# Optimization experiments

Hardware: AMD Instinct MI355X
Metric: run time of the kernel (lower is better)

## Reference

```python
import jax, jax.numpy as jnp
import numpy as np

EMBED = 1024
HEADS = 16
HEAD_DIM = EMBED // HEADS
EPS = 1e-5  # torch LayerNorm default


def setup_inputs() -> dict:
    key = jax.random.key(0)
    ks = jax.random.split(key, 11)
    s = 1.0 / np.sqrt(EMBED)
    def lin(kw, kb):
        W = jax.random.uniform(kw, (EMBED, EMBED), jnp.float32, -s, s)
        b = jax.random.uniform(kb, (EMBED,), jnp.float32, -s, s)
        return W, b
    Wq, bq = lin(ks[0], ks[1])
    Wk, bk = lin(ks[2], ks[3])
    Wv, bv = lin(ks[4], ks[5])
    Wo, bo = lin(ks[6], ks[7])
    x = jax.random.normal(ks[8], (2, 2048, EMBED), jnp.float32)
    gamma = jnp.ones((EMBED,), jnp.float32)
    beta = jnp.zeros((EMBED,), jnp.float32)
    return {"x": x, "Wq": Wq, "bq": bq, "Wk": Wk, "bk": bk,
            "Wv": Wv, "bv": bv, "Wo": Wo, "bo": bo,
            "gamma": gamma, "beta": beta}


def _attn(x, Wq, bq, Wk, bk, Wv, bv, Wo, bo, gamma, beta):
    N, S, _ = x.shape
    # torch Linear: y = x @ W.T + b
    q = (x @ Wq.T + bq).reshape(N, S, HEADS, HEAD_DIM).transpose(0, 2, 1, 3)
    k = (x @ Wk.T + bk).reshape(N, S, HEADS, HEAD_DIM).transpose(0, 2, 1, 3)
    v = (x @ Wv.T + bv).reshape(N, S, HEADS, HEAD_DIM).transpose(0, 2, 1, 3)
    energy = jnp.einsum("bhqd,bhkd->bhqk", q, k) / np.sqrt(HEAD_DIM)
    causal = jnp.tril(jnp.ones((S, S), bool))  # [S,S]
    energy = jnp.where(causal[None, None], energy, -jnp.inf)
    attn = jax.nn.softmax(energy, axis=-1)
    out = jnp.einsum("bhqk,bhkd->bhqd", attn, v)
    out = out.transpose(0, 2, 1, 3).reshape(N, S, EMBED)
    out = out @ Wo.T + bo
    # residual + LayerNorm
    h = out + x
    mu = jnp.mean(h, axis=-1, keepdims=True)
    var = jnp.var(h, axis=-1, keepdims=True)
    return (h - mu) * jax.lax.rsqrt(var + EPS) * gamma + beta


def reference(x, Wq, bq, Wk, bk, Wv, bv, Wo, bo, gamma, beta):
    return _attn(x, Wq, bq, Wk, bk, Wv, bv, Wo, bo, gamma, beta)
```

## Files before the change

### kernel.cpp

```cpp
#include <hip/hip_runtime.h>

typedef __attribute__((ext_vector_type(8))) short short8;
typedef __attribute__((ext_vector_type(4))) float f32x4;
typedef __attribute__((ext_vector_type(4))) short short4v;

template<bool B> struct BoolC { static constexpr bool value = B; };

__device__ __forceinline__ short f2bs(float f) {
    union { float f; unsigned u; } c; c.f = f;
    unsigned r = 0x7FFFu + ((c.u >> 16) & 1u);
    return (short)((c.u + r) >> 16);
}

__device__ __forceinline__ unsigned fbits(float f) {
    union { float f; unsigned u; } c; c.f = f; return c.u;
}

__device__ __forceinline__ float fast_exp2(float x) {
    float r;
    asm("v_exp_f32 %0, %1" : "=v"(r) : "v"(x));
    return r;
}

__device__ __forceinline__ void gld_lds16(const void* g, void* l) {
    __builtin_amdgcn_global_load_lds(
        (const __attribute__((address_space(1))) unsigned int*)g,
        (__attribute__((address_space(3))) unsigned int*)l, 16, 0, 0);
}

__device__ __forceinline__ f32x4 mfma16(short8 a, short8 b, f32x4 c) {
    return __builtin_amdgcn_mfma_f32_16x16x32_bf16(a, b, c, 0, 0, 0);
}

template<int N> __device__ __forceinline__ void vmwait() {
    if constexpr (N == 0)      asm volatile("s_waitcnt vmcnt(0)" ::: "memory");
    else if constexpr (N == 3) asm volatile("s_waitcnt vmcnt(3)" ::: "memory");
    else if constexpr (N == 4) asm volatile("s_waitcnt vmcnt(4)" ::: "memory");
}

__global__ __launch_bounds__(256) void cvtall_kernel(
    const float* __restrict__ x,
    const float* __restrict__ Wq, const float* __restrict__ Wk,
    const float* __restrict__ Wv, const float* __restrict__ Wo,
    short* __restrict__ xb, short* __restrict__ wqkv, short* __restrict__ wob)
{
    int i = blockIdx.x * 256 + threadIdx.x;
    const float* src; short* dst; int off;
    if (i < 1048576) { src = x; dst = xb; off = i; }
    else {
        int j = i - 1048576, which = j >> 18;
        off = j & 262143;
        src = which == 0 ? Wq : (which == 1 ? Wk : (which == 2 ? Wv : Wo));
        dst = which == 3 ? wob : (wqkv + (size_t)which * 1048576);
    }
    float4 v = ((const float4*)src)[off];
    short4v o;
    o.x = f2bs(v.x); o.y = f2bs(v.y); o.z = f2bs(v.z); o.w = f2bs(v.w);
    ((short4v*)dst)[off] = o;
}

#define BN 128
#define BK 32

template<int MODE, int BMt>
__global__ __launch_bounds__(256) void gemm_bt(
    const short* __restrict__ A, const short* __restrict__ B,
    int M, int N, int K,
    const float* __restrict__ b0, const float* __restrict__ b1, const float* __restrict__ b2,
    short* __restrict__ oq, short* __restrict__ ok_, short* __restrict__ ov,
    const float* __restrict__ bo, const float* __restrict__ xres,
    float* __restrict__ outf)
{
    constexpr int IM = BMt / 32;
    constexpr int BUFSZ = (BMt + BN) * BK;
    constexpr int LPS = (BMt == 128) ? 4 : 3;
    __shared__ __align__(16) short SM[3 * BUFSZ];
    const int tid = threadIdx.x;
    const int wave = tid >> 6, lane = tid & 63;
    const int lhi = lane >> 4, llo = lane & 15;
    const int row0 = blockIdx.x * BMt, col0 = blockIdx.y * BN;
    const int wr = (wave >> 1) * (BMt / 2), wc = (wave & 1) * 64;

    f32x4 acc[IM][4] = {};

    const short* gA0 = A + (size_t)(row0 + (tid >> 2)) * K + (tid & 3) * 8;
    const short* gA1 = A + (size_t)(row0 + 64 + (tid >> 2)) * K + (tid & 3) * 8;
    const short* gB0 = B + (size_t)(col0 + (tid >> 2)) * K + (tid & 3) * 8;
    const short* gB1 = B + (size_t)(col0 + 64 + (tid >> 2)) * K + (tid & 3) * 8;

    auto stage = [&](int kk, int bf) {
        short* As = SM + bf * BUFSZ;
        short* Bs = As + BMt * BK;
        gld_lds16(gA0 + kk, &As[wave * 512]);
        if constexpr (BMt == 128) gld_lds16(gA1 + kk, &As[2048 + wave * 512]);
        gld_lds16(gB0 + kk, &Bs[wave * 512]);
        gld_lds16(gB1 + kk, &Bs[2048 + wave * 512]);
    };

    const int NT = K / BK;
    stage(0, 0);
    stage(BK, 1);

    for (int kt = 0; kt < NT; ++kt) {
        if (kt < NT - 1) vmwait<LPS>(); else vmwait<0>();
        __builtin_amdgcn_s_barrier();
        __builtin_amdgcn_sched_barrier(0);
        if (kt + 2 < NT) stage((kt + 2) * BK, (kt + 2) % 3);
        const short* As = SM + (kt % 3) * BUFSZ;
        const short* Bs = As + BMt * BK;
        short8 af[IM], bfr[4];
        #pragma unroll
        for (int i = 0; i < IM; ++i)
            af[i] = *(const short8*)&As[(wr + i * 16 + llo) * BK + lhi * 8];
        #pragma unroll
        for (int j = 0; j < 4; ++j)
            bfr[j] = *(const short8*)&Bs[(wc + j * 16 + llo) * BK + lhi * 8];
        #pragma unroll
        for (int i = 0; i < IM; ++i)
            #pragma unroll
            for (int j = 0; j < 4; ++j)
                acc[i][j] = mfma16(af[i], bfr[j], acc[i][j]);
    }

    if constexpr (MODE == 0) {
        const int which = (int)blockIdx.y >> 3;
        if (which < 2) {
            const float* bia = which == 0 ? b0 : b1;
            short* dst = which == 0 ? oq : ok_;
            #pragma unroll
            for (int i = 0; i < IM; ++i)
                #pragma unroll
                for (int j = 0; j < 4; ++j)
                    #pragma unroll
                    for (int r = 0; r < 4; ++r) {
                        int m = row0 + wr + i * 16 + lhi * 4 + r;
                        int nn = (col0 & 1023) + wc + j * 16 + llo;
                        float v = acc[i][j][r] + bia[nn];
                        int h = nn >> 6, d = nn & 63;
                        int bb = m >> 11, s = m & 2047;
                        dst[((size_t)((bb * 16 + h) * 2048 + s)) * 64 + d] = f2bs(v);
                    }
        } else {
            __syncthreads();
            short* T = SM + wave * (64 * 26);
            const int nn0 = (col0 - 2048) + wc;
            const int h = nn0 >> 6;
            const int bb = row0 >> 11;
            const int s0 = (row0 & 2047) + wr;
            short* vdst = ov + ((size_t)(bb * 16 + h) * 64) * 2048;
            #pragma unroll
            for (int i = 0; i < IM; ++i) {
                #pragma unroll
                for (int j = 0; j < 4; ++j) {
                    const float bias = b2[nn0 + j * 16 + llo];
                    unsigned u01 = __builtin_amdgcn_perm(fbits(acc[i][j][1] + bias),
                                                         fbits(acc[i][j][0] + bias), 0x07060302u);
                    unsigned u23 = __builtin_amdgcn_perm(fbits(acc[i][j][3] + bias),
                                                         fbits(acc[i][j][2] + bias), 0x07060302u);
                    unsigned* Tw = (unsigned*)&T[(j * 16 + llo) * 26];
                    Tw[lhi * 2]     = u01;
                    Tw[lhi * 2 + 1] = u23;
                }
                short8 a0 = *(const short8*)&T[lane * 26];
                short8 a1 = *(const short8*)&T[lane * 26 + 8];
                *(short8*)&vdst[(size_t)lane * 2048 + s0 + i * 16]     = a0;
                *(short8*)&vdst[(size_t)lane * 2048 + s0 + i * 16 + 8] = a1;
            }
        }
    } else {
        #pragma unroll
        for (int i = 0; i < IM; ++i)
            #pragma unroll
            for (int j = 0; j < 4; ++j)
                #pragma unroll
                for (int r = 0; r < 4; ++r) {
                    int m = row0 + wr + i * 16 + lhi * 4 + r;
                    int n = col0 + wc + j * 16 + llo;
                    size_t idx = (size_t)m * N + n;
                    outf[idx] = acc[i][j][r] + bo[n] + xres[idx];
                }
    }
}

#define SCL 0.18033688011f

__global__ __launch_bounds__(256) void attn_kernel(
    const short* __restrict__ Q, const short* __restrict__ K,
    const short* __restrict__ Vt, short* __restrict__ O)
{
    const int id = blockIdx.x;
    const int u = id >> 3;
    const int bh = (id & 7) * 4 + (u & 3);
    const int s4 = u >> 2;
    const int p = (s4 < 8) ? (2 * s4) : (31 - 2 * s4);
    const int q0L = p * 64, q0H = (31 - p) * 64;
    const int ntH = 32 - p;

    const short* Qb = Q  + (size_t)bh * 2048 * 64;
    const short* Kb = K  + (size_t)bh * 2048 * 64;
    const short* Vb = Vt + (size_t)bh * 64 * 2048;

    __shared__ __align__(16) short Ks[2][64 * 64];
    __shared__ __align__(16) short Vs[2][64 * 64];
    __shared__ __align__(16) short Ps[4][2][16 * 68];

    const int tid = threadIdx.x, wave = tid >> 6, lane = tid & 63;
    const int lhi = lane >> 4, llo = lane & 15;
    const int qwL = q0L + wave * 16, qwH = q0H + wave * 16;
    const int qgL = qwL + llo, qgH = qwH + llo;

    auto scale8 = [](short8 a) {
        short8 r;
        #pragma unroll
        for (int i = 0; i < 8; ++i) {
            union { unsigned u; float f; } c; c.u = ((unsigned)(unsigned short)a[i]) << 16;
            r[i] = f2bs(c.f * SCL);
        }
        return r;
    };
    const short8 qfL0 = scale8(*(const short8*)&Qb[(size_t)(qwL + llo) * 64 + lhi * 8]);
    const short8 qfL1 = scale8(*(const short8*)&Qb[(size_t)(qwL + llo) * 64 + 32 + lhi * 8]);
    const short8 qfH0 = scale8(*(const short8*)&Qb[(size_t)(qwH + llo) * 64 + lhi * 8]);
    const short8 qfH1 = scale8(*(const short8*)&Qb[(size_t)(qwH + llo) * 64 + 32 + lhi * 8]);

    const int tr = tid >> 3, tc = tid & 7, sc = tc ^ (tr & 7);
    const short* kS0 = Kb + (size_t)tr * 64 + sc * 8;
    const short* kS1 = Kb + (size_t)(32 + tr) * 64 + sc * 8;
    const short* vS0 = Vb + (size_t)tr * 2048 + sc * 8;
    const short* vS1 = Vb + (size_t)(32 + tr) * 2048 + sc * 8;
    const int dOff = wave * 512;

    f32x4 oL[4] = {}, oH[4] = {};
    float lL = 0.f, lH = 0.f;

    unsigned* PwH = (unsigned*)Ps[wave][0] + llo * 34;
    unsigned* PwL = (unsigned*)Ps[wave][1] + llo * 34;

    gld_lds16(kS0, Ks[0] + dOff);
    gld_lds16(kS1, Ks[0] + 2048 + dOff);
    gld_lds16(vS0, Vs[0] + dOff);
    gld_lds16(vS1, Vs[0] + 2048 + dOff);
    __syncthreads();

    const int swq = (llo & 7) << 3;

    auto smx = [&](f32x4 (&st)[4], float& lrow, unsigned* Pw, int qg, int kk0, bool diag) {
        if (diag) {
            #pragma unroll
            for (int t = 0; t < 4; ++t)
                #pragma unroll
                for (int j = 0; j < 4; ++j)
                    if (kk0 + t * 16 + lhi * 4 + j > qg) st[t][j] = -1e30f;
        }
        float rs0 = 0.f, rs1 = 0.f;
        #pragma unroll
        for (int t = 0; t < 4; ++t) {
            st[t][0] = fast_exp2(st[t][0]);
            st[t][1] = fast_exp2(st[t][1]);
            st[t][2] = fast_exp2(st[t][2]);
            st[t][3] = fast_exp2(st[t][3]);
            rs0 += st[t][0] + st[t][2];
            rs1 += st[t][1] + st[t][3];
        }
        lrow += rs0 + rs1;
        #pragma unroll
        for (int t = 0; t < 4; ++t) {
            Pw[t * 8 + lhi * 2]     = __builtin_amdgcn_perm(fbits(st[t][1]), fbits(st[t][0]), 0x07060302u);
            Pw[t * 8 + lhi * 2 + 1] = __builtin_amdgcn_perm(fbits(st[t][3]), fbits(st[t][2]), 0x07060302u);
        }
    };

    int cur = 0;
    auto tile = [&](int kt, auto dualc) {
        constexpr bool DUAL = decltype(dualc)::value;
        const int kk0 = kt * 64;
        if (kt + 1 < ntH) {
            const int nk = kk0 + 64;
            gld_lds16(kS0 + (size_t)nk * 64, Ks[cur ^ 1] + dOff);
            gld_lds16(kS1 + (size_t)nk * 64, Ks[cur ^ 1] + 2048 + dOff);
            gld_lds16(vS0 + nk, Vs[cur ^ 1] + dOff);
            gld_lds16(vS1 + nk, Vs[cur ^ 1] + 2048 + dOff);
        }

        f32x4 stH[4], stL[4];
        __builtin_amdgcn_s_setprio(1);
        #pragma unroll
        for (int t = 0; t < 4; ++t) {
            const int row = t * 16 + llo;
            short8 kf0 = *(const short8*)&Ks[cur][row * 64 + ((lhi * 8) ^ swq)];
            short8 kf1 = *(const short8*)&Ks[cur][row * 64 + ((lhi * 8 + 32) ^ swq)];
            f32x4 a = {};
            a = mfma16(kf0, qfH0, a);
            stH[t] = mfma16(kf1, qfH1, a);
            if (DUAL) {
                f32x4 b = {};
                b = mfma16(kf0, qfL0, b);
                stL[t] = mfma16(kf1, qfL1, b);
            }
        }
        __builtin_amdgcn_s_setprio(0);

        smx(stH, lH, PwH, qgH, kk0, kt == ntH - 1);
        if (DUAL) smx(stL, lL, PwL, qgL, kk0, kt == p);

        const short8 pH0 = *(const short8*)&Ps[wave][0][llo * 68 + lhi * 8];
        const short8 pH1 = *(const short8*)&Ps[wave][0][llo * 68 + 32 + lhi * 8];
        short8 pL0, pL1;
        if (DUAL) {
            pL0 = *(const short8*)&Ps[wave][1][llo * 68 + lhi * 8];
            pL1 = *(const short8*)&Ps[wave][1][llo * 68 + 32 + lhi * 8];
        }
        __builtin_amdgcn_s_setprio(1);
        #pragma unroll
        for (int dt = 0; dt < 4; ++dt) {
            const int row = dt * 16 + llo;
            short8 vf0 = *(const short8*)&Vs[cur][row * 64 + ((lhi * 8) ^ swq)];
            short8 vf1 = *(const short8*)&Vs[cur][row * 64 + ((lhi * 8 + 32) ^ swq)];
            oH[dt] = mfma16(pH0, vf0, oH[dt]);
            oH[dt] = mfma16(pH1, vf1, oH[dt]);
            if (DUAL) {
                oL[dt] = mfma16(pL0, vf0, oL[dt]);
                oL[dt] = mfma16(pL1, vf1, oL[dt]);
            }
        }
        __builtin_amdgcn_s_setprio(0);

        if (kt + 1 < ntH) __syncthreads();
        cur ^= 1;
    };

    for (int kt = 0; kt <= p; ++kt)      tile(kt, BoolC<true>{});
    for (int kt = p + 1; kt < ntH; ++kt) tile(kt, BoolC<false>{});

    lH += __shfl_xor(lH, 16); lH += __shfl_xor(lH, 32);
    lL += __shfl_xor(lL, 16); lL += __shfl_xor(lL, 32);
    const int b = bh >> 4, h = bh & 15;
    const float invH = 1.f / lH, invL = 1.f / lL;
    #pragma unroll
    for (int j = 0; j < 4; ++j) {
        const float ivH = __shfl(invH, lhi * 4 + j);
        const float ivL = __shfl(invL, lhi * 4 + j);
        const size_t rowH = (size_t)(b * 2048 + qwH + lhi * 4 + j);
        const size_t rowL = (size_t)(b * 2048 + qwL + lhi * 4 + j);
        #pragma unroll
        for (int dt = 0; dt < 4; ++dt) {
            int d = dt * 16 + llo;
            O[rowH * 1024 + h * 64 + d] = f2bs(oH[dt][j] * ivH);
            O[rowL * 1024 + h * 64 + d] = f2bs(oL[dt][j] * ivL);
        }
    }
}

__global__ __launch_bounds__(256) void ln_kernel(float* __restrict__ out,
        const float* __restrict__ gamma, const float* __restrict__ beta)
{
    const int row = blockIdx.x;
    float* p = out + (size_t)row * 1024;
    const int tid = threadIdx.x;
    float4 v = ((const float4*)p)[tid];
    float s = v.x + v.y + v.z + v.w;
    float ss = v.x * v.x + v.y * v.y + v.z * v.z + v.w * v.w;
    #pragma unroll
    for (int d = 1; d < 64; d <<= 1) {
        s  += __shfl_xor(s, d);
        ss += __shfl_xor(ss, d);
    }
    __shared__ float red[8];
    const int wave = tid >> 6, lane = tid & 63;
    if (lane == 0) { red[wave] = s; red[4 + wave] = ss; }
    __syncthreads();
    s  = red[0] + red[1] + red[2] + red[3];
    ss = red[4] + red[5] + red[6] + red[7];
    const float mu = s * (1.0f / 1024.0f);
    const float var = ss * (1.0f / 1024.0f) - mu * mu;
    const float rstd = rsqrtf(var + 1e-5f);
    float4 g = ((const float4*)gamma)[tid];
    float4 b = ((const float4*)beta)[tid];
    v.x = (v.x - mu) * rstd * g.x + b.x;
    v.y = (v.y - mu) * rstd * g.y + b.y;
    v.z = (v.z - mu) * rstd * g.z + b.z;
    v.w = (v.w - mu) * rstd * g.w + b.w;
    ((float4*)p)[tid] = v;
}

extern "C" void kernel_launch(void* const* d_in, const int* in_sizes, int n_in,
                              void* d_out, int out_size, void* d_ws, size_t ws_size,
                              hipStream_t stream)
{
    const float* x  = (const float*)d_in[0];
    const float* Wq = (const float*)d_in[1];
    const float* bq = (const float*)d_in[2];
    const float* Wk = (const float*)d_in[3];
    const float* bk = (const float*)d_in[4];
    const float* Wv = (const float*)d_in[5];
    const float* bv = (const float*)d_in[6];
    const float* Wo = (const float*)d_in[7];
    const float* bo = (const float*)d_in[8];
    const float* gamma = (const float*)d_in[9];
    const float* beta  = (const float*)d_in[10];
    float* out = (float*)d_out;

    char* ws = (char*)d_ws;
    short* xb   = (short*)(ws);
    short* wqkv = (short*)(ws + (8ull  << 20));
    short* wob  = (short*)(ws + (14ull << 20));
    short* qb   = (short*)(ws + (16ull << 20));
    short* kb   = (short*)(ws + (24ull << 20));
    short* vtb  = (short*)(ws + (32ull << 20));
    short* ab   = xb;

    cvtall_kernel<<<8192, 256, 0, stream>>>(x, Wq, Wk, Wv, Wo, xb, wqkv, wob);

    gemm_bt<0, 128><<<dim3(32, 24), 256, 0, stream>>>(xb, wqkv, 4096, 3072, 1024,
        bq, bk, bv, qb, kb, vtb, nullptr, nullptr, nullptr);

    attn_kernel<<<512, 256, 0, stream>>>(qb, kb, vtb, ab);

    gemm_bt<1, 64><<<dim3(64, 8), 256, 0, stream>>>(ab, wob, 4096, 1024, 1024,
        nullptr, nullptr, nullptr, nullptr, nullptr, nullptr, bo, x, out);

    ln_kernel<<<4096, 256, 0, stream>>>(out, gamma, beta);
}
```

Baseline: 111.2 us.

## Restructure attention to one query tile per block with split-K wave partitioning

Replaces the paired low/high query-tile scheduling (512 blocks) with one 64-row query tile per block (1024 blocks, heaviest tiles first). Within a block, waves split the work 2x2 across key halves and query halves, keep P in registers instead of staging through LDS, and combine the partial outputs and row sums through shared memory at the end. The intent is more parallelism and no per-tile LDS round-trip for P. In exchange it adds a cross-wave reduction and more blocks with uneven work.

```diff
diff --git a/kernel.cpp b/kernel.cpp
--- a/kernel.cpp
+++ b/kernel.cpp
@@ -3,8 +3,6 @@
 typedef __attribute__((ext_vector_type(8))) short short8;
 typedef __attribute__((ext_vector_type(4))) float f32x4;
 typedef __attribute__((ext_vector_type(4))) short short4v;
-
-template<bool B> struct BoolC { static constexpr bool value = B; };
 
 __device__ __forceinline__ short f2bs(float f) {
     union { float f; unsigned u; } c; c.f = f;
@@ -189,25 +187,23 @@
     const short* __restrict__ Vt, short* __restrict__ O)
 {
     const int id = blockIdx.x;
-    const int u = id >> 3;
-    const int bh = (id & 7) * 4 + (u & 3);
-    const int s4 = u >> 2;
-    const int p = (s4 < 8) ? (2 * s4) : (31 - 2 * s4);
-    const int q0L = p * 64, q0H = (31 - p) * 64;
-    const int ntH = 32 - p;
+    const int bh = (id & 7) * 4 + (id >> 8);
+    const int qt = 31 - ((id >> 3) & 31);
+    const int q0 = qt * 64;
+    const int nt = qt + 1;
 
     const short* Qb = Q  + (size_t)bh * 2048 * 64;
     const short* Kb = K  + (size_t)bh * 2048 * 64;
     const short* Vb = Vt + (size_t)bh * 64 * 2048;
 
-    __shared__ __align__(16) short Ks[2][64 * 64];
-    __shared__ __align__(16) short Vs[2][64 * 64];
-    __shared__ __align__(16) short Ps[4][2][16 * 68];
+    __shared__ __align__(16) short SMEM[4 * 4096];
+    __shared__ float Lred[2][64];
+    short* Ksb = SMEM;
+    short* Vsb = SMEM + 2 * 4096;
 
     const int tid = threadIdx.x, wave = tid >> 6, lane = tid & 63;
     const int lhi = lane >> 4, llo = lane & 15;
-    const int qwL = q0L + wave * 16, qwH = q0H + wave * 16;
-    const int qgL = qwL + llo, qgH = qwH + llo;
+    const int kh = wave >> 1, qh = wave & 1;
 
     auto scale8 = [](short8 a) {
         short8 r;
@@ -218,10 +214,12 @@
         }
         return r;
     };
-    const short8 qfL0 = scale8(*(const short8*)&Qb[(size_t)(qwL + llo) * 64 + lhi * 8]);
-    const short8 qfL1 = scale8(*(const short8*)&Qb[(size_t)(qwL + llo) * 64 + 32 + lhi * 8]);
-    const short8 qfH0 = scale8(*(const short8*)&Qb[(size_t)(qwH + llo) * 64 + lhi * 8]);
-    const short8 qfH1 = scale8(*(const short8*)&Qb[(size_t)(qwH + llo) * 64 + 32 + lhi * 8]);
+    short8 qf[2][2];
+    #pragma unroll
+    for (int qs = 0; qs < 2; ++qs)
+        #pragma unroll
+        for (int h = 0; h < 2; ++h)
+            qf[qs][h] = scale8(*(const short8*)&Qb[(size_t)(q0 + qh * 32 + qs * 16 + llo) * 64 + h * 32 + lhi * 8]);
 
     const int tr = tid >> 3, tc = tid & 7, sc = tc ^ (tr & 7);
     const short* kS0 = Kb + (size_t)tr * 64 + sc * 8;
@@ -230,125 +228,124 @@
     const short* vS1 = Vb + (size_t)(32 + tr) * 2048 + sc * 8;
     const int dOff = wave * 512;
 
-    f32x4 oL[4] = {}, oH[4] = {};
-    float lL = 0.f, lH = 0.f;
-
-    unsigned* PwH = (unsigned*)Ps[wave][0] + llo * 34;
-    unsigned* PwL = (unsigned*)Ps[wave][1] + llo * 34;
-
-    gld_lds16(kS0, Ks[0] + dOff);
-    gld_lds16(kS1, Ks[0] + 2048 + dOff);
-    gld_lds16(vS0, Vs[0] + dOff);
-    gld_lds16(vS1, Vs[0] + 2048 + dOff);
+    f32x4 o[4][2] = {};
+    float lp[2] = {0.f, 0.f};
+
+    gld_lds16(kS0, Ksb + dOff);
+    gld_lds16(kS1, Ksb + 2048 + dOff);
+    gld_lds16(vS0, Vsb + dOff);
+    gld_lds16(vS1, Vsb + 2048 + dOff);
     __syncthreads();
 
-    const int swq = (llo & 7) << 3;
-
-    auto smx = [&](f32x4 (&st)[4], float& lrow, unsigned* Pw, int qg, int kk0, bool diag) {
-        if (diag) {
-            #pragma unroll
-            for (int t = 0; t < 4; ++t)
+    const int gbase = kh * 32 + ((llo & 12) << 1) + (llo & 3);
+    const int vrow = 0;
+
+    int cur = 0;
+    for (int kt = 0; kt < nt; ++kt) {
+        const int kk0 = kt * 64;
+        if (kt + 1 < nt) {
+            const int nk = kk0 + 64;
+            gld_lds16(kS0 + (size_t)nk * 64, Ksb + (cur ^ 1) * 4096 + dOff);
+            gld_lds16(kS1 + (size_t)nk * 64, Ksb + (cur ^ 1) * 4096 + 2048 + dOff);
+            gld_lds16(vS0 + nk, Vsb + (cur ^ 1) * 4096 + dOff);
+            gld_lds16(vS1 + nk, Vsb + (cur ^ 1) * 4096 + 2048 + dOff);
+        }
+
+        const short* Kc = Ksb + cur * 4096;
+        const short* Vc = Vsb + cur * 4096;
+        f32x4 st[2][2];
+        __builtin_amdgcn_s_setprio(1);
+        #pragma unroll
+        for (int s = 0; s < 2; ++s) {
+            const int g = gbase + s * 4;
+            const int sw = (g & 7) << 3;
+            short8 kf0 = *(const short8*)&Kc[g * 64 + ((lhi * 8) ^ sw)];
+            short8 kf1 = *(const short8*)&Kc[g * 64 + ((lhi * 8 + 32) ^ sw)];
+            #pragma unroll
+            for (int qs = 0; qs < 2; ++qs) {
+                f32x4 a = {};
+                a = mfma16(kf0, qf[qs][0], a);
+                st[s][qs] = mfma16(kf1, qf[qs][1], a);
+            }
+        }
+        __builtin_amdgcn_s_setprio(0);
+
+        if (kt == nt - 1) {
+            #pragma unroll
+            for (int s = 0; s < 2; ++s)
                 #pragma unroll
-                for (int j = 0; j < 4; ++j)
-                    if (kk0 + t * 16 + lhi * 4 + j > qg) st[t][j] = -1e30f;
-        }
-        float rs0 = 0.f, rs1 = 0.f;
-        #pragma unroll
-        for (int t = 0; t < 4; ++t) {
-            st[t][0] = fast_exp2(st[t][0]);
-            st[t][1] = fast_exp2(st[t][1]);
-            st[t][2] = fast_exp2(st[t][2]);
-            st[t][3] = fast_exp2(st[t][3]);
-            rs0 += st[t][0] + st[t][2];
-            rs1 += st[t][1] + st[t][3];
-        }
-        lrow += rs0 + rs1;
-        #pragma unroll
-        for (int t = 0; t < 4; ++t) {
-            Pw[t * 8 + lhi * 2]     = __builtin_amdgcn_perm(fbits(st[t][1]), fbits(st[t][0]), 0x07060302u);
-            Pw[t * 8 + lhi * 2 + 1] = __builtin_amdgcn_perm(fbits(st[t][3]), fbits(st[t][2]), 0x07060302u);
-        }
-    };
-
-    int cur = 0;
-    auto tile = [&](int kt, auto dualc) {
-        constexpr bool DUAL = decltype(dualc)::value;
-        const int kk0 = kt * 64;
-        if (kt + 1 < ntH) {
-            const int nk = kk0 + 64;
-            gld_lds16(kS0 + (size_t)nk * 64, Ks[cur ^ 1] + dOff);
-            gld_lds16(kS1 + (size_t)nk * 64, Ks[cur ^ 1] + 2048 + dOff);
-            gld_lds16(vS0 + nk, Vs[cur ^ 1] + dOff);
-            gld_lds16(vS1 + nk, Vs[cur ^ 1] + 2048 + dOff);
-        }
-
-        f32x4 stH[4], stL[4];
+                for (int qs = 0; qs < 2; ++qs)
+                    #pragma unroll
+                    for (int j = 0; j < 4; ++j)
+                        if (kk0 + kh * 32 + lhi * 8 + s * 4 + j > q0 + qh * 32 + qs * 16 + llo)
+                            st[s][qs][j] = -1e30f;
+        }
+
+        short8 pb[2];
+        #pragma unroll
+        for (int qs = 0; qs < 2; ++qs) {
+            #pragma unroll
+            for (int s = 0; s < 2; ++s)
+                #pragma unroll
+                for (int j = 0; j < 4; ++j) {
+                    st[s][qs][j] = fast_exp2(st[s][qs][j]);
+                    lp[qs] += st[s][qs][j];
+                }
+            union { short8 s8; unsigned u[4]; } pk;
+            pk.u[0] = __builtin_amdgcn_perm(fbits(st[0][qs][1]), fbits(st[0][qs][0]), 0x07060302u);
+            pk.u[1] = __builtin_amdgcn_perm(fbits(st[0][qs][3]), fbits(st[0][qs][2]), 0x07060302u);
+            pk.u[2] = __builtin_amdgcn_perm(fbits(st[1][qs][1]), fbits(st[1][qs][0]), 0x07060302u);
+            pk.u[3] = __builtin_amdgcn_perm(fbits(st[1][qs][3]), fbits(st[1][qs][2]), 0x07060302u);
+            pb[qs] = pk.s8;
+        }
+
         __builtin_amdgcn_s_setprio(1);
         #pragma unroll
-        for (int t = 0; t < 4; ++t) {
-            const int row = t * 16 + llo;
-            short8 kf0 = *(const short8*)&Ks[cur][row * 64 + ((lhi * 8) ^ swq)];
-            short8 kf1 = *(const short8*)&Ks[cur][row * 64 + ((lhi * 8 + 32) ^ swq)];
-            f32x4 a = {};
-            a = mfma16(kf0, qfH0, a);
-            stH[t] = mfma16(kf1, qfH1, a);
-            if (DUAL) {
-                f32x4 b = {};
-                b = mfma16(kf0, qfL0, b);
-                stL[t] = mfma16(kf1, qfL1, b);
-            }
+        for (int ds = 0; ds < 4; ++ds) {
+            const int row = ds * 16 + llo;
+            const int sw = (row & 7) << 3;
+            short8 vf = *(const short8*)&Vc[row * 64 + ((kh * 32 + lhi * 8) ^ sw)];
+            o[ds][0] = mfma16(vf, pb[0], o[ds][0]);
+            o[ds][1] = mfma16(vf, pb[1], o[ds][1]);
         }
         __builtin_amdgcn_s_setprio(0);
 
-        smx(stH, lH, PwH, qgH, kk0, kt == ntH - 1);
-        if (DUAL) smx(stL, lL, PwL, qgL, kk0, kt == p);
-
-        const short8 pH0 = *(const short8*)&Ps[wave][0][llo * 68 + lhi * 8];
-        const short8 pH1 = *(const short8*)&Ps[wave][0][llo * 68 + 32 + lhi * 8];
-        short8 pL0, pL1;
-        if (DUAL) {
-            pL0 = *(const short8*)&Ps[wave][1][llo * 68 + lhi * 8];
-            pL1 = *(const short8*)&Ps[wave][1][llo * 68 + 32 + lhi * 8];
-        }
-        __builtin_amdgcn_s_setprio(1);
-        #pragma unroll
-        for (int dt = 0; dt < 4; ++dt) {
-            const int row = dt * 16 + llo;
-            short8 vf0 = *(const short8*)&Vs[cur][row * 64 + ((lhi * 8) ^ swq)];
-            short8 vf1 = *(const short8*)&Vs[cur][row * 64 + ((lhi * 8 + 32) ^ swq)];
-            oH[dt] = mfma16(pH0, vf0, oH[dt]);
-            oH[dt] = mfma16(pH1, vf1, oH[dt]);
-            if (DUAL) {
-                oL[dt] = mfma16(pL0, vf0, oL[dt]);
-                oL[dt] = mfma16(pL1, vf1, oL[dt]);
-            }
-        }
-        __builtin_amdgcn_s_setprio(0);
-
-        if (kt + 1 < ntH) __syncthreads();
+        if (kt + 1 < nt) __syncthreads();
         cur ^= 1;
-    };
-
-    for (int kt = 0; kt <= p; ++kt)      tile(kt, BoolC<true>{});
-    for (int kt = p + 1; kt < ntH; ++kt) tile(kt, BoolC<false>{});
-
-    lH += __shfl_xor(lH, 16); lH += __shfl_xor(lH, 32);
-    lL += __shfl_xor(lL, 16); lL += __shfl_xor(lL, 32);
+    }
+
+    #pragma unroll
+    for (int qs = 0; qs < 2; ++qs) {
+        float lq = lp[qs];
+        lq += __shfl_xor(lq, 16);
+        lq += __shfl_xor(lq, 32);
+        if (lhi == 0) Lred[kh][qh * 32 + qs * 16 + llo] = lq;
+    }
+    __syncthreads();
+
+    float* OredF = (float*)SMEM;
+    #pragma unroll
+    for (int ds = 0; ds < 4; ++ds)
+        #pragma unroll
+        for (int qs = 0; qs < 2; ++qs)
+            #pragma unroll
+            for (int r = 0; r < 4; ++r)
+                OredF[kh * 4096 + (ds * 16 + lhi * 4 + r) * 64 + qh * 32 + qs * 16 + llo] = o[ds][qs][r];
+    __syncthreads();
+
     const int b = bh >> 4, h = bh & 15;
-    const float invH = 1.f / lH, invL = 1.f / lL;
+    const int qq = tid >> 2, dg = tid & 3;
+    const float linv = 1.f / (Lred[0][qq] + Lred[1][qq]);
+    short vout[16];
     #pragma unroll
-    for (int j = 0; j < 4; ++j) {
-        const float ivH = __shfl(invH, lhi * 4 + j);
-        const float ivL = __shfl(invL, lhi * 4 + j);
-        const size_t rowH = (size_t)(b * 2048 + qwH + lhi * 4 + j);
-        const size_t rowL = (size_t)(b * 2048 + qwL + lhi * 4 + j);
-        #pragma unroll
-        for (int dt = 0; dt < 4; ++dt) {
-            int d = dt * 16 + llo;
-            O[rowH * 1024 + h * 64 + d] = f2bs(oH[dt][j] * ivH);
-            O[rowL * 1024 + h * 64 + d] = f2bs(oL[dt][j] * ivL);
-        }
-    }
+    for (int dd = 0; dd < 16; ++dd) {
+        const int d = dg * 16 + dd;
+        float v = OredF[d * 64 + qq] + OredF[4096 + d * 64 + qq];
+        vout[dd] = f2bs(v * linv);
+    }
+    short* dst = O + ((size_t)(b * 2048 + q0 + qq)) * 1024 + h * 64 + dg * 16;
+    *(short8*)dst       = *(short8*)&vout[0];
+    *(short8*)(dst + 8) = *(short8*)&vout[8];
 }
 
 __global__ __launch_bounds__(256) void ln_kernel(float* __restrict__ out,
@@ -414,7 +411,7 @@
     gemm_bt<0, 128><<<dim3(32, 24), 256, 0, stream>>>(xb, wqkv, 4096, 3072, 1024,
         bq, bk, bv, qb, kb, vtb, nullptr, nullptr, nullptr);
 
-    attn_kernel<<<512, 256, 0, stream>>>(qb, kb, vtb, ab);
+    attn_kernel<<<1024, 256, 0, stream>>>(qb, kb, vtb, ab);
 
     gemm_bt<1, 64><<<dim3(64, 8), 256, 0, stream>>>(ab, wob, 4096, 1024, 1024,
         nullptr, nullptr, nullptr, nullptr, nullptr, nullptr, bo, x, out);
```

Result: slower. 119.6 us (+7.6%).
